# Kernel optimization log

Hardware: AMD Instinct MI355X
Metric: run time of the kernel (lower is better)

The kernel has to match this reference:

```python
import jax, jax.numpy as jnp
import numpy as np

B, C, H, W = 8, 64, 256, 256
DW = 2 * C          # dw_channel
FFN = 2 * C         # ffn_channel
EPS = 1e-6


def setup_inputs() -> dict:
    key = jax.random.key(0)
    ks = jax.random.split(key, 16)
    f = lambda k, s, scale=1.0: (jax.random.normal(k, s, jnp.float32) * scale)
    return {
        "inp": f(ks[0], (B, C, H, W)),
        "w1": f(ks[1], (B, DW, C, 1, 1)),
        "b1": f(ks[2], (B, DW), 0.01),
        "w2": f(ks[3], (B, DW, 1, 3, 3)),
        "b2": f(ks[4], (B, DW), 0.01),
        "w3": f(ks[5], (B, C, DW // 2, 1, 1)),
        "b3": f(ks[6], (B, C), 0.01),
        "w4": f(ks[7], (B, FFN, C, 1, 1)),
        "b4": f(ks[8], (B, FFN), 0.01),
        "w5": f(ks[9], (B, C, FFN // 2, 1, 1)),
        "b5": f(ks[10], (B, C), 0.01),
        "ln1_w": jnp.ones((C,), jnp.float32),
        "ln1_b": jnp.zeros((C,), jnp.float32),
        "ln2_w": jnp.ones((C,), jnp.float32),
        "ln2_b": jnp.zeros((C,), jnp.float32),
        "sca_w": f(ks[11], (DW // 2, DW // 2, 1, 1), 0.05),
        "sca_b": jnp.zeros((DW // 2,), jnp.float32),
        "beta": f(ks[12], (1, C, 1, 1), 0.1),
        "gamma": f(ks[13], (1, C, 1, 1), 0.1),
    }


def _layernorm2d(x, w, b):
    # LayerNorm over channel dim per pixel (NAFNet LayerNorm2d)
    mu = jnp.mean(x, axis=1, keepdims=True)
    var = jnp.var(x, axis=1, keepdims=True)
    xn = (x - mu) * jax.lax.rsqrt(var + EPS)
    return xn * w[None, :, None, None] + b[None, :, None, None]


def _normalize_weights(w):
    # w: [B, co, ci, kh, kw]; Frobenius norm over (ci, kh, kw) per (b, co)
    nrm = jnp.sqrt(jnp.sum(w * w, axis=(2, 3, 4), keepdims=True))
    return w / nrm


def _pw(x, w, b):
    # per-sample 1x1 conv: x [B,ci,H,W], w [B,co,ci,1,1], b [B,co]
    return jnp.einsum("bchw,boc->bohw", x, w[:, :, :, 0, 0]) + b[:, :, None, None]


def _dw3x3(x, w, b):
    # per-sample depthwise 3x3: x [B,DW,H,W], w [B,DW,1,3,3], b [B,DW]
    def one(xi, wi):
        y = jax.lax.conv_general_dilated(
            xi[None], wi, window_strides=(1, 1), padding="SAME",
            dimension_numbers=("NCHW", "OIHW", "NCHW"),
            feature_group_count=DW)
        return y[0]
    return jax.vmap(one)(x, w) + b[:, :, None, None]


def _simple_gate(x):
    x1, x2 = jnp.split(x, 2, axis=1)
    return x1 * x2


def reference(inp, w1, b1, w2, b2, w3, b3, w4, b4, w5, b5,
              ln1_w, ln1_b, ln2_w, ln2_b, sca_w, sca_b, beta, gamma):
    x = _layernorm2d(inp, ln1_w, ln1_b)
    x = _pw(x, _normalize_weights(w1), b1)          # [B,DW,H,W]
    x = _dw3x3(x, _normalize_weights(w2), b2)       # [B,DW,H,W]
    x = _simple_gate(x)                             # [B,DW/2,H,W]
    pooled = jnp.mean(x, axis=(2, 3))               # [B,DW/2]
    sca = jnp.einsum("bc,oc->bo", pooled, sca_w[:, :, 0, 0]) + sca_b
    x = x * sca[:, :, None, None]
    x = _pw(x, _normalize_weights(w3), b3)          # [B,C,H,W]
    y = inp + x * beta
    x = _layernorm2d(y, ln2_w, ln2_b)
    x = _pw(x, _normalize_weights(w4), b4)          # [B,FFN,H,W]
    x = _simple_gate(x)                             # [B,FFN/2,H,W]
    x = _pw(x, _normalize_weights(w5), b5)          # [B,C,H,W]
    return y + x * gamma
```

## Files before the change

### kernel.cpp

```cpp
#include <hip/hip_runtime.h>
#include <hip/hip_bf16.h>

typedef __attribute__((ext_vector_type(8))) short short8;
typedef __attribute__((ext_vector_type(4))) float f32x4;

#define HWN 65536
#define WN 256
#define HN 256

#define TW 32
#define TH 8
#define HALO_W 34
#define HALO_N 340
#define MT_N 22

#define W2N_OFF 0
#define W1BF_OFF 9216
#define W3BF_OFF 41984
#define W4BF_OFF 58368
#define W5BF_OFF 91136
#define POOL_OFF 107520
#define SCA_OFF 108032

static __device__ __forceinline__ short f2bs(float f) {
    union { __hip_bfloat16 h; short s; } u; u.h = __float2bfloat16(f); return u.s;
}
static __device__ __forceinline__ float bs2f(short s) {
    union { unsigned u; float f; } v; v.u = ((unsigned)(unsigned short)s) << 16; return v.f;
}

__device__ __forceinline__ void norm_row(const float* __restrict__ in,
                                         float* __restrict__ out, int n) {
    float s = 0.f;
    for (int i = 0; i < n; i++) { float v = in[i]; s += v * v; }
    float r = rsqrtf(s);
    for (int i = 0; i < n; i++) out[i] = in[i] * r;
}

__device__ __forceinline__ void norm_row_bf(const float* __restrict__ in,
                                            short* __restrict__ out, int n) {
    float s = 0.f;
    for (int i = 0; i < n; i++) { float v = in[i]; s += v * v; }
    float r = rsqrtf(s);
    for (int i = 0; i < n; i++) out[i] = f2bs(in[i] * r);
}

__global__ void k_prep(const float* __restrict__ w1, const float* __restrict__ w2,
                       const float* __restrict__ w3, const float* __restrict__ w4,
                       const float* __restrict__ w5, float* __restrict__ ws) {
    int r = blockIdx.x * 256 + threadIdx.x;
    short* w1bf = (short*)(ws + W1BF_OFF);
    short* w3bf = (short*)(ws + W3BF_OFF);
    short* w4bf = (short*)(ws + W4BF_OFF);
    short* w5bf = (short*)(ws + W5BF_OFF);
    if (r < 1024) {
        norm_row_bf(w1 + r * 64, w1bf + r * 64, 64);
    } else if (r < 2048) {
        int rr = r - 1024;
        norm_row(w2 + rr * 9, ws + W2N_OFF + rr * 9, 9);
    } else if (r < 2560) {
        int rr = r - 2048;
        norm_row_bf(w3 + rr * 64, w3bf + rr * 64, 64);
    } else if (r < 3584) {
        int rr = r - 2560;
        norm_row_bf(w4 + rr * 64, w4bf + rr * 64, 64);
    } else if (r < 4096) {
        int rr = r - 3584;
        norm_row_bf(w5 + rr * 64, w5bf + rr * 64, 64);
    } else if (r < 4608) {
        ws[POOL_OFF + (r - 4096)] = 0.f;
    }
}

__global__ __launch_bounds__(256, 3) void k1(
    const float* __restrict__ inp, const float* __restrict__ ln1w,
    const float* __restrict__ ln1b, const float* __restrict__ b1,
    const float* __restrict__ b2v, const float* __restrict__ ws,
    float* __restrict__ g, float* __restrict__ pooled) {
    const short* w1bf = (const short*)(ws + W1BF_OFF);
    const float* w2n = ws + W2N_OFF;
    const int b = blockIdx.x >> 8;
    const int tile = blockIdx.x & 255;
    const int x0 = (tile & 7) << 5, y0 = (tile >> 3) << 3;
    const int t = threadIdx.x;
    const int wave = t >> 6, lane = t & 63;
    const int n = lane & 15, q = lane >> 4;

    __shared__ short sPA[2][HALO_N * 8];
    __shared__ short sPB[2][HALO_N * 8];
    __shared__ float sRed[8 * 4 * 8];

    float wc[16], bc[16];
#pragma unroll
    for (int j = 0; j < 8; j++) {
        wc[j] = ln1w[q * 8 + j];
        bc[j] = ln1b[q * 8 + j];
        wc[8 + j] = ln1w[32 + q * 8 + j];
        bc[8 + j] = ln1b[32 + q * 8 + j];
    }

    short8 afr0[6], afr1[6];
    const float* xb = inp + ((size_t)b << 22);
#pragma unroll
    for (int i = 0; i < 6; i++) {
        int mt = wave + i * 4;
        if (mt < MT_N) {
            int pix = mt * 16 + n;
            int hy = pix / HALO_W, hx = pix - hy * HALO_W;
            int yy = y0 - 1 + hy, xx = x0 - 1 + hx;
            bool inb = ((unsigned)yy < HN) && ((unsigned)xx < WN) && (pix < HALO_N);
            const float* xin = xb + (yy * WN + xx);
            float x[16];
            float s = 0.f, s2 = 0.f;
#pragma unroll
            for (int j = 0; j < 8; j++) {
                float v0 = inb ? xin[(size_t)(q * 8 + j) << 16] : 0.f;
                float v1 = inb ? xin[(size_t)(32 + q * 8 + j) << 16] : 0.f;
                x[j] = v0; x[8 + j] = v1;
                s += v0 + v1; s2 += v0 * v0 + v1 * v1;
            }
            s += __shfl_xor(s, 16); s += __shfl_xor(s, 32);
            s2 += __shfl_xor(s2, 16); s2 += __shfl_xor(s2, 32);
            float mu = s * (1.f / 64.f);
            float var = s2 * (1.f / 64.f) - mu * mu;
            float rr = rsqrtf(var + 1e-6f);
            short8 a0, a1;
#pragma unroll
            for (int j = 0; j < 8; j++) {
                a0[j] = f2bs((x[j] - mu) * rr * wc[j] + bc[j]);
                a1[j] = f2bs((x[8 + j] - mu) * rr * wc[8 + j] + bc[8 + j]);
            }
            afr0[i] = a0; afr1[i] = a1;
        }
    }

    unsigned vmask = 0;
#pragma unroll
    for (int i = 0; i < 6; i++) {
        int mt = wave + i * 4;
        if (mt < MT_N) {
#pragma unroll
            for (int r = 0; r < 4; r++) {
                int row = mt * 16 + q * 4 + r;
                int hy = row / HALO_W, hx = row - hy * HALO_W;
                int yy = y0 - 1 + hy, xx = x0 - 1 + hx;
                if (row < HALO_N && ((unsigned)yy < HN) && ((unsigned)xx < WN))
                    vmask |= 1u << (i * 4 + r);
            }
        }
    }

    const short* w1b = w1bf + b * 128 * 64;
    const float* w2b = w2n + b * 128 * 9;
    const float* b1b = b1 + b * 128;
    const float* b2b = b2v + b * 128;
    const int lx = t & 31, ly = t >> 5;

    for (int cc = 0; cc < 8; cc++) {
        int outch = cc * 8 + (n < 8 ? n : 56 + n);
        short8 bf0 = *(const short8*)(w1b + outch * 64 + q * 8);
        short8 bf1 = *(const short8*)(w1b + outch * 64 + 32 + q * 8);
        float bias = b1b[outch];
        short* spA = sPA[cc & 1];
        short* spB = sPB[cc & 1];
#pragma unroll
        for (int i = 0; i < 6; i++) {
            int mt = wave + i * 4;
            if (mt < MT_N) {
                f32x4 d = {0.f, 0.f, 0.f, 0.f};
                d = __builtin_amdgcn_mfma_f32_16x16x32_bf16(afr0[i], bf0, d, 0, 0, 0);
                d = __builtin_amdgcn_mfma_f32_16x16x32_bf16(afr1[i], bf1, d, 0, 0, 0);
#pragma unroll
                for (int r = 0; r < 4; r++) {
                    int row = mt * 16 + q * 4 + r;
                    short val = ((vmask >> (i * 4 + r)) & 1u) ? f2bs(d[r] + bias)
                                                              : (short)0;
                    if (row < HALO_N) {
                        if (n < 8) spA[row * 8 + n] = val;
                        else       spB[row * 8 + (n - 8)] = val;
                    }
                }
            }
        }
        __syncthreads();
        float accA[8], accB[8];
#pragma unroll
        for (int p = 0; p < 8; p++) {
            accA[p] = b2b[cc * 8 + p];
            accB[p] = b2b[64 + cc * 8 + p];
        }
#pragma unroll
        for (int ky = 0; ky < 3; ky++) {
#pragma unroll
            for (int kx = 0; kx < 3; kx++) {
                int e = (ly + ky) * HALO_W + lx + kx;
                short8 pA = *(const short8*)&spA[e * 8];
                short8 pB = *(const short8*)&spB[e * 8];
#pragma unroll
                for (int p = 0; p < 8; p++) {
                    accA[p] += bs2f(pA[p]) * w2b[(cc * 8 + p) * 9 + ky * 3 + kx];
                    accB[p] += bs2f(pB[p]) * w2b[(64 + cc * 8 + p) * 9 + ky * 3 + kx];
                }
            }
        }
        float v[8];
        size_t gbase = ((size_t)(b * 64 + cc * 8)) * HWN + (size_t)((y0 + ly) * WN + x0 + lx);
#pragma unroll
        for (int p = 0; p < 8; p++) {
            v[p] = accA[p] * accB[p];
            g[gbase + ((size_t)p << 16)] = v[p];
        }
#pragma unroll
        for (int p = 0; p < 8; p++) {
            float s = v[p];
            s += __shfl_xor(s, 1);  s += __shfl_xor(s, 2);
            s += __shfl_xor(s, 4);  s += __shfl_xor(s, 8);
            s += __shfl_xor(s, 16); s += __shfl_xor(s, 32);
            if (lane == 0) sRed[(cc * 4 + wave) * 8 + p] = s;
        }
    }
    __syncthreads();
    if (t < 64) {
        int cc = t >> 3, p = t & 7;
        float s = sRed[(cc * 4 + 0) * 8 + p] + sRed[(cc * 4 + 1) * 8 + p] +
                  sRed[(cc * 4 + 2) * 8 + p] + sRed[(cc * 4 + 3) * 8 + p];
        atomicAdd(&pooled[b * 64 + cc * 8 + p], s);
    }
}

__global__ void k_sca(const float* __restrict__ pooled,
                      const float* __restrict__ scaw,
                      const float* __restrict__ scab,
                      float* __restrict__ sca) {
    int t = threadIdx.x;
    int b = t >> 6, o = t & 63;
    float acc = scab[o];
    for (int c = 0; c < 64; c++)
        acc += pooled[b * 64 + c] * (1.f / 65536.f) * scaw[o * 64 + c];
    sca[t] = acc;
}

__global__ __launch_bounds__(256, 4) void k2(
    const float* __restrict__ inp, const float* g, const float* __restrict__ ws,
    const float* __restrict__ b3, const float* __restrict__ beta,
    const float* __restrict__ ln2w, const float* __restrict__ ln2b,
    const float* __restrict__ b4, const float* __restrict__ b5,
    const float* __restrict__ gamma, float* out) {
    const int b = blockIdx.x >> 9;
    const int px0 = (blockIdx.x & 511) << 7;
    const int t = threadIdx.x;
    const int wave = t >> 6, lane = t & 63;
    const int n = lane & 15, q = lane >> 4;

    __shared__ short sX[128 * 72];
    __shared__ short sB[128 * 72];

    const float* scav = ws + SCA_OFF + b * 64;

    {
        const float* gb = g + ((size_t)b << 22) + px0;
        for (int i = t; i < 128 * 64; i += 256) {
            int c = i >> 7, px = i & 127;
            sX[px * 72 + c] = f2bs(gb[((size_t)c << 16) + px] * scav[c]);
        }
    }
    __syncthreads();

    float yreg[4][2][4];
    {
        const short* w3b = (const short*)(ws + W3BF_OFF) + b * 64 * 64;
        const float* b3b = b3 + b * 64;
#pragma unroll
        for (int nc = 0; nc < 4; nc++) {
            int outch = nc * 16 + n;
            short8 bf0 = *(const short8*)(w3b + outch * 64 + q * 8);
            short8 bf1 = *(const short8*)(w3b + outch * 64 + 32 + q * 8);
            float b3v = b3b[outch], betav = beta[outch];
            const float* ib = inp + ((size_t)b << 22) + ((size_t)outch << 16) + px0;
#pragma unroll
            for (int mi = 0; mi < 2; mi++) {
                int mt = wave + mi * 4;
                const short* arow = &sX[(mt * 16 + n) * 72];
                short8 a0 = *(const short8*)(arow + q * 8);
                short8 a1 = *(const short8*)(arow + 32 + q * 8);
                f32x4 d = {0.f, 0.f, 0.f, 0.f};
                d = __builtin_amdgcn_mfma_f32_16x16x32_bf16(a0, bf0, d, 0, 0, 0);
                d = __builtin_amdgcn_mfma_f32_16x16x32_bf16(a1, bf1, d, 0, 0, 0);
                f32x4 resid = *(const f32x4*)(ib + mt * 16 + q * 4);
#pragma unroll
                for (int r = 0; r < 4; r++) {
                    float y = resid[r] + betav * (d[r] + b3v);
                    yreg[nc][mi][r] = y;
                    sB[(mt * 16 + q * 4 + r) * 72 + outch] = f2bs(y);
                }
            }
        }
    }
    __syncthreads();

    {
        int px = t >> 1, half = t & 1;
        const short* yrow = &sB[px * 72 + half * 32];
        short8 yv[4];
        float s = 0.f, s2 = 0.f;
#pragma unroll
        for (int v8 = 0; v8 < 4; v8++) {
            yv[v8] = *(const short8*)(yrow + v8 * 8);
#pragma unroll
            for (int j = 0; j < 8; j++) {
                float f = bs2f(yv[v8][j]);
                s += f; s2 += f * f;
            }
        }
        s += __shfl_xor(s, 1); s2 += __shfl_xor(s2, 1);
        float mu = s * (1.f / 64.f);
        float var = s2 * (1.f / 64.f) - mu * mu;
        float rr = rsqrtf(var + 1e-6f);
        short* xrow = &sX[px * 72 + half * 32];
#pragma unroll
        for (int v8 = 0; v8 < 4; v8++) {
            short8 o;
#pragma unroll
            for (int j = 0; j < 8; j++) {
                int c = half * 32 + v8 * 8 + j;
                o[j] = f2bs((bs2f(yv[v8][j]) - mu) * rr * ln2w[c] + ln2b[c]);
            }
            *(short8*)(xrow + v8 * 8) = o;
        }
    }
    __syncthreads();

    {
        const short* w4b = (const short*)(ws + W4BF_OFF) + b * 128 * 64;
        const float* b4b = b4 + b * 128;
        for (int cc = 0; cc < 8; cc++) {
            int outch = cc * 8 + (n < 8 ? n : 56 + n);
            short8 bf0 = *(const short8*)(w4b + outch * 64 + q * 8);
            short8 bf1 = *(const short8*)(w4b + outch * 64 + 32 + q * 8);
            float b4v = b4b[outch];
#pragma unroll
            for (int mi = 0; mi < 2; mi++) {
                int mt = wave + mi * 4;
                const short* arow = &sX[(mt * 16 + n) * 72];
                short8 a0 = *(const short8*)(arow + q * 8);
                short8 a1 = *(const short8*)(arow + 32 + q * 8);
                f32x4 d = {0.f, 0.f, 0.f, 0.f};
                d = __builtin_amdgcn_mfma_f32_16x16x32_bf16(a0, bf0, d, 0, 0, 0);
                d = __builtin_amdgcn_mfma_f32_16x16x32_bf16(a1, bf1, d, 0, 0, 0);
#pragma unroll
                for (int r = 0; r < 4; r++) {
                    float val = d[r] + b4v;
                    float other = __shfl_xor(val, 8);
                    if (n < 8)
                        sB[(mt * 16 + q * 4 + r) * 72 + cc * 8 + n] = f2bs(val * other);
                }
            }
        }
    }
    __syncthreads();

    {
        const short* w5b = (const short*)(ws + W5BF_OFF) + b * 64 * 64;
        const float* b5b = b5 + b * 64;
        float* ob = out + ((size_t)b << 22) + px0;
#pragma unroll
        for (int nc = 0; nc < 4; nc++) {
            int outch = nc * 16 + n;
            short8 bf0 = *(const short8*)(w5b + outch * 64 + q * 8);
            short8 bf1 = *(const short8*)(w5b + outch * 64 + 32 + q * 8);
            float b5v = b5b[outch], gam = gamma[outch];
#pragma unroll
            for (int mi = 0; mi < 2; mi++) {
                int mt = wave + mi * 4;
                const short* arow = &sB[(mt * 16 + n) * 72];
                short8 a0 = *(const short8*)(arow + q * 8);
                short8 a1 = *(const short8*)(arow + 32 + q * 8);
                f32x4 d = {0.f, 0.f, 0.f, 0.f};
                d = __builtin_amdgcn_mfma_f32_16x16x32_bf16(a0, bf0, d, 0, 0, 0);
                d = __builtin_amdgcn_mfma_f32_16x16x32_bf16(a1, bf1, d, 0, 0, 0);
                f32x4 o;
#pragma unroll
                for (int r = 0; r < 4; r++)
                    o[r] = yreg[nc][mi][r] + gam * (d[r] + b5v);
                *(f32x4*)(ob + ((size_t)outch << 16) + mt * 16 + q * 4) = o;
            }
        }
    }
}

extern "C" void kernel_launch(void* const* d_in, const int* in_sizes, int n_in,
                              void* d_out, int out_size, void* d_ws, size_t ws_size,
                              hipStream_t stream) {
    const float* inp  = (const float*)d_in[0];
    const float* w1   = (const float*)d_in[1];
    const float* b1   = (const float*)d_in[2];
    const float* w2   = (const float*)d_in[3];
    const float* b2v  = (const float*)d_in[4];
    const float* w3   = (const float*)d_in[5];
    const float* b3   = (const float*)d_in[6];
    const float* w4   = (const float*)d_in[7];
    const float* b4   = (const float*)d_in[8];
    const float* w5   = (const float*)d_in[9];
    const float* b5   = (const float*)d_in[10];
    const float* ln1w = (const float*)d_in[11];
    const float* ln1b = (const float*)d_in[12];
    const float* ln2w = (const float*)d_in[13];
    const float* ln2b = (const float*)d_in[14];
    const float* scaw = (const float*)d_in[15];
    const float* scab = (const float*)d_in[16];
    const float* beta = (const float*)d_in[17];
    const float* gamma= (const float*)d_in[18];

    float* ws = (float*)d_ws;
    float* pooled = ws + POOL_OFF;
    float* sca = ws + SCA_OFF;
    float* g = (float*)d_out;
    float* out = (float*)d_out;

    k_prep<<<17, 256, 0, stream>>>(w1, w2, w3, w4, w5, ws);
    k1<<<2048, 256, 0, stream>>>(inp, ln1w, ln1b, b1, b2v, ws, g, pooled);
    k_sca<<<1, 512, 0, stream>>>(pooled, scaw, scab, sca);
    k2<<<4096, 256, 0, stream>>>(inp, g, ws, b3, beta, ln2w, ln2b, b4, b5,
                                 gamma, out);
}
```

Baseline: 533.0 us.

## Store depthwise staging in fp32, pipeline input loads, vectorize g loads, hoist MFMA A fragments

The k1 depthwise staging buffers change from bf16 to fp32. This drops the bf16 convert on store and the unpack on read, but doubles LDS use, which may lower occupancy under launch_bounds(256,3). The input load and LayerNorm loop is software-pipelined with two register buffers so global loads overlap with compute. In the second kernel, g is loaded as float4 vectors, and the MFMA A fragments are hoisted out of the output-channel loops so they are read from LDS once.

```diff
diff --git a/kernel.cpp b/kernel.cpp
--- a/kernel.cpp
+++ b/kernel.cpp
@@ -8,8 +8,6 @@
 #define WN 256
 #define HN 256
 
-#define TW 32
-#define TH 8
 #define HALO_W 34
 #define HALO_N 340
 #define MT_N 22
@@ -86,8 +84,8 @@
     const int wave = t >> 6, lane = t & 63;
     const int n = lane & 15, q = lane >> 4;
 
-    __shared__ short sPA[2][HALO_N * 8];
-    __shared__ short sPB[2][HALO_N * 8];
+    __shared__ float sPA[2][HALO_N * 8];
+    __shared__ float sPB[2][HALO_N * 8];
     __shared__ float sRed[8 * 4 * 8];
 
     float wc[16], bc[16];
@@ -100,39 +98,57 @@
     }
 
     short8 afr0[6], afr1[6];
-    const float* xb = inp + ((size_t)b << 22);
-#pragma unroll
-    for (int i = 0; i < 6; i++) {
-        int mt = wave + i * 4;
-        if (mt < MT_N) {
-            int pix = mt * 16 + n;
-            int hy = pix / HALO_W, hx = pix - hy * HALO_W;
-            int yy = y0 - 1 + hy, xx = x0 - 1 + hx;
-            bool inb = ((unsigned)yy < HN) && ((unsigned)xx < WN) && (pix < HALO_N);
-            const float* xin = xb + (yy * WN + xx);
-            float x[16];
-            float s = 0.f, s2 = 0.f;
-#pragma unroll
-            for (int j = 0; j < 8; j++) {
-                float v0 = inb ? xin[(size_t)(q * 8 + j) << 16] : 0.f;
-                float v1 = inb ? xin[(size_t)(32 + q * 8 + j) << 16] : 0.f;
-                x[j] = v0; x[8 + j] = v1;
-                s += v0 + v1; s2 += v0 * v0 + v1 * v1;
-            }
-            s += __shfl_xor(s, 16); s += __shfl_xor(s, 32);
-            s2 += __shfl_xor(s2, 16); s2 += __shfl_xor(s2, 32);
-            float mu = s * (1.f / 64.f);
-            float var = s2 * (1.f / 64.f) - mu * mu;
-            float rr = rsqrtf(var + 1e-6f);
-            short8 a0, a1;
-#pragma unroll
-            for (int j = 0; j < 8; j++) {
-                a0[j] = f2bs((x[j] - mu) * rr * wc[j] + bc[j]);
-                a1[j] = f2bs((x[8 + j] - mu) * rr * wc[8 + j] + bc[8 + j]);
-            }
-            afr0[i] = a0; afr1[i] = a1;
-        }
-    }
+    const float* xbase = inp + ((size_t)b << 22);
+    float va[16], vb[16];
+
+#define LOADX(dst, I)                                                         \
+    if (wave + (I) * 4 < MT_N) {                                              \
+        int pix = (wave + (I) * 4) * 16 + n;                                  \
+        int hy = pix / HALO_W, hx = pix - hy * HALO_W;                        \
+        int yy = y0 - 1 + hy, xx = x0 - 1 + hx;                               \
+        bool inb = ((unsigned)yy < HN) && ((unsigned)xx < WN) &&              \
+                   (pix < HALO_N);                                            \
+        const float* xin = xbase + (yy * WN + xx);                            \
+        _Pragma("unroll")                                                     \
+        for (int j = 0; j < 8; j++) {                                         \
+            dst[j]     = inb ? xin[(size_t)(q * 8 + j) << 16] : 0.f;          \
+            dst[8 + j] = inb ? xin[(size_t)(32 + q * 8 + j) << 16] : 0.f;     \
+        }                                                                     \
+    }
+
+#define LNX(src, I)                                                           \
+    if (wave + (I) * 4 < MT_N) {                                              \
+        float s = 0.f, s2 = 0.f;                                              \
+        _Pragma("unroll")                                                     \
+        for (int j = 0; j < 16; j++) { s += src[j]; s2 += src[j] * src[j]; }  \
+        s += __shfl_xor(s, 16); s += __shfl_xor(s, 32);                       \
+        s2 += __shfl_xor(s2, 16); s2 += __shfl_xor(s2, 32);                   \
+        float mu = s * (1.f / 64.f);                                          \
+        float var = s2 * (1.f / 64.f) - mu * mu;                              \
+        float rr = rsqrtf(var + 1e-6f);                                       \
+        short8 a0, a1;                                                        \
+        _Pragma("unroll")                                                     \
+        for (int j = 0; j < 8; j++) {                                         \
+            a0[j] = f2bs((src[j] - mu) * rr * wc[j] + bc[j]);                 \
+            a1[j] = f2bs((src[8 + j] - mu) * rr * wc[8 + j] + bc[8 + j]);     \
+        }                                                                     \
+        afr0[(I)] = a0; afr1[(I)] = a1;                                       \
+    }
+
+    LOADX(va, 0)
+    LOADX(vb, 1)
+    LNX(va, 0)
+    LOADX(va, 2)
+    LNX(vb, 1)
+    LOADX(vb, 3)
+    LNX(va, 2)
+    LOADX(va, 4)
+    LNX(vb, 3)
+    LOADX(vb, 5)
+    LNX(va, 4)
+    LNX(vb, 5)
+#undef LOADX
+#undef LNX
 
     unsigned vmask = 0;
 #pragma unroll
@@ -161,8 +177,8 @@
         short8 bf0 = *(const short8*)(w1b + outch * 64 + q * 8);
         short8 bf1 = *(const short8*)(w1b + outch * 64 + 32 + q * 8);
         float bias = b1b[outch];
-        short* spA = sPA[cc & 1];
-        short* spB = sPB[cc & 1];
+        float* spA = sPA[cc & 1];
+        float* spB = sPB[cc & 1];
 #pragma unroll
         for (int i = 0; i < 6; i++) {
             int mt = wave + i * 4;
@@ -173,8 +189,7 @@
 #pragma unroll
                 for (int r = 0; r < 4; r++) {
                     int row = mt * 16 + q * 4 + r;
-                    short val = ((vmask >> (i * 4 + r)) & 1u) ? f2bs(d[r] + bias)
-                                                              : (short)0;
+                    float val = ((vmask >> (i * 4 + r)) & 1u) ? (d[r] + bias) : 0.f;
                     if (row < HALO_N) {
                         if (n < 8) spA[row * 8 + n] = val;
                         else       spB[row * 8 + (n - 8)] = val;
@@ -194,12 +209,18 @@
 #pragma unroll
             for (int kx = 0; kx < 3; kx++) {
                 int e = (ly + ky) * HALO_W + lx + kx;
-                short8 pA = *(const short8*)&spA[e * 8];
-                short8 pB = *(const short8*)&spB[e * 8];
-#pragma unroll
-                for (int p = 0; p < 8; p++) {
-                    accA[p] += bs2f(pA[p]) * w2b[(cc * 8 + p) * 9 + ky * 3 + kx];
-                    accB[p] += bs2f(pB[p]) * w2b[(64 + cc * 8 + p) * 9 + ky * 3 + kx];
+                f32x4 a0v = *(const f32x4*)&spA[e * 8];
+                f32x4 a1v = *(const f32x4*)&spA[e * 8 + 4];
+                f32x4 b0v = *(const f32x4*)&spB[e * 8];
+                f32x4 b1v = *(const f32x4*)&spB[e * 8 + 4];
+                const float* wA = w2b + (cc * 8) * 9 + ky * 3 + kx;
+                const float* wB = w2b + (64 + cc * 8) * 9 + ky * 3 + kx;
+#pragma unroll
+                for (int p = 0; p < 4; p++) {
+                    accA[p]     += a0v[p] * wA[p * 9];
+                    accA[p + 4] += a1v[p] * wA[(p + 4) * 9];
+                    accB[p]     += b0v[p] * wB[p * 9];
+                    accB[p + 4] += b1v[p] * wB[(p + 4) * 9];
                 }
             }
         }
@@ -259,9 +280,13 @@
 
     {
         const float* gb = g + ((size_t)b << 22) + px0;
-        for (int i = t; i < 128 * 64; i += 256) {
-            int c = i >> 7, px = i & 127;
-            sX[px * 72 + c] = f2bs(gb[((size_t)c << 16) + px] * scav[c]);
+        for (int i2 = t; i2 < 2048; i2 += 256) {
+            int c = i2 >> 5, pxg = i2 & 31;
+            f32x4 v = *(const f32x4*)&gb[((size_t)c << 16) + pxg * 4];
+            float sc = scav[c];
+#pragma unroll
+            for (int r = 0; r < 4; r++)
+                sX[(pxg * 4 + r) * 72 + c] = f2bs(v[r] * sc);
         }
     }
     __syncthreads();
@@ -270,6 +295,13 @@
     {
         const short* w3b = (const short*)(ws + W3BF_OFF) + b * 64 * 64;
         const float* b3b = b3 + b * 64;
+        short8 a0h[2], a1h[2];
+#pragma unroll
+        for (int mi = 0; mi < 2; mi++) {
+            const short* arow = &sX[((wave + mi * 4) * 16 + n) * 72];
+            a0h[mi] = *(const short8*)(arow + q * 8);
+            a1h[mi] = *(const short8*)(arow + 32 + q * 8);
+        }
 #pragma unroll
         for (int nc = 0; nc < 4; nc++) {
             int outch = nc * 16 + n;
@@ -280,12 +312,9 @@
 #pragma unroll
             for (int mi = 0; mi < 2; mi++) {
                 int mt = wave + mi * 4;
-                const short* arow = &sX[(mt * 16 + n) * 72];
-                short8 a0 = *(const short8*)(arow + q * 8);
-                short8 a1 = *(const short8*)(arow + 32 + q * 8);
                 f32x4 d = {0.f, 0.f, 0.f, 0.f};
-                d = __builtin_amdgcn_mfma_f32_16x16x32_bf16(a0, bf0, d, 0, 0, 0);
-                d = __builtin_amdgcn_mfma_f32_16x16x32_bf16(a1, bf1, d, 0, 0, 0);
+                d = __builtin_amdgcn_mfma_f32_16x16x32_bf16(a0h[mi], bf0, d, 0, 0, 0);
+                d = __builtin_amdgcn_mfma_f32_16x16x32_bf16(a1h[mi], bf1, d, 0, 0, 0);
                 f32x4 resid = *(const f32x4*)(ib + mt * 16 + q * 4);
 #pragma unroll
                 for (int r = 0; r < 4; r++) {
@@ -333,6 +362,13 @@
     {
         const short* w4b = (const short*)(ws + W4BF_OFF) + b * 128 * 64;
         const float* b4b = b4 + b * 128;
+        short8 a0h[2], a1h[2];
+#pragma unroll
+        for (int mi = 0; mi < 2; mi++) {
+            const short* arow = &sX[((wave + mi * 4) * 16 + n) * 72];
+            a0h[mi] = *(const short8*)(arow + q * 8);
+            a1h[mi] = *(const short8*)(arow + 32 + q * 8);
+        }
         for (int cc = 0; cc < 8; cc++) {
             int outch = cc * 8 + (n < 8 ? n : 56 + n);
             short8 bf0 = *(const short8*)(w4b + outch * 64 + q * 8);
@@ -341,12 +377,9 @@
 #pragma unroll
             for (int mi = 0; mi < 2; mi++) {
                 int mt = wave + mi * 4;
-                const short* arow = &sX[(mt * 16 + n) * 72];
-                short8 a0 = *(const short8*)(arow + q * 8);
-                short8 a1 = *(const short8*)(arow + 32 + q * 8);
                 f32x4 d = {0.f, 0.f, 0.f, 0.f};
-                d = __builtin_amdgcn_mfma_f32_16x16x32_bf16(a0, bf0, d, 0, 0, 0);
-                d = __builtin_amdgcn_mfma_f32_16x16x32_bf16(a1, bf1, d, 0, 0, 0);
+                d = __builtin_amdgcn_mfma_f32_16x16x32_bf16(a0h[mi], bf0, d, 0, 0, 0);
+                d = __builtin_amdgcn_mfma_f32_16x16x32_bf16(a1h[mi], bf1, d, 0, 0, 0);
 #pragma unroll
                 for (int r = 0; r < 4; r++) {
                     float val = d[r] + b4v;
@@ -363,6 +396,13 @@
         const short* w5b = (const short*)(ws + W5BF_OFF) + b * 64 * 64;
         const float* b5b = b5 + b * 64;
         float* ob = out + ((size_t)b << 22) + px0;
+        short8 a0h[2], a1h[2];
+#pragma unroll
+        for (int mi = 0; mi < 2; mi++) {
+            const short* arow = &sB[((wave + mi * 4) * 16 + n) * 72];
+            a0h[mi] = *(const short8*)(arow + q * 8);
+            a1h[mi] = *(const short8*)(arow + 32 + q * 8);
+        }
 #pragma unroll
         for (int nc = 0; nc < 4; nc++) {
             int outch = nc * 16 + n;
@@ -372,12 +412,9 @@
 #pragma unroll
             for (int mi = 0; mi < 2; mi++) {
                 int mt = wave + mi * 4;
-                const short* arow = &sB[(mt * 16 + n) * 72];
-                short8 a0 = *(const short8*)(arow + q * 8);
-                short8 a1 = *(const short8*)(arow + 32 + q * 8);
                 f32x4 d = {0.f, 0.f, 0.f, 0.f};
-                d = __builtin_amdgcn_mfma_f32_16x16x32_bf16(a0, bf0, d, 0, 0, 0);
-                d = __builtin_amdgcn_mfma_f32_16x16x32_bf16(a1, bf1, d, 0, 0, 0);
+                d = __builtin_amdgcn_mfma_f32_16x16x32_bf16(a0h[mi], bf0, d, 0, 0, 0);
+                d = __builtin_amdgcn_mfma_f32_16x16x32_bf16(a1h[mi], bf1, d, 0, 0, 0);
                 f32x4 o;
 #pragma unroll
                 for (int r = 0; r < 4; r++)
```

Measured after the change: 608.8 us. 1.14x slower.
